# Performance work log

Hardware: AMD Instinct MI355X
Metric: run time of the kernel (lower is better)

## Reference

```python
import jax, jax.numpy as jnp
import numpy as np

B, SQ, SK = 2, 2048, 4096
D_STATE, D_LISTEN, D_PROJ, H = 512, 512, 512, 8


def setup_inputs() -> dict:
    key = jax.random.key(0)
    ks = jax.random.split(key, 9)
    s = 0.02
    return {
        "q": jax.random.normal(ks[0], (B, SQ, D_STATE), jnp.float32),
        "k": jax.random.normal(ks[1], (B, SK, D_LISTEN), jnp.float32),
        "mask": jax.random.randint(ks[2], (B, SK), 0, 2, jnp.int32),
        "Wq": jax.random.normal(ks[3], (D_STATE, D_PROJ), jnp.float32) * s,
        "bq": jnp.zeros((D_PROJ,), jnp.float32),
        "Wk": jax.random.normal(ks[4], (D_LISTEN, D_PROJ), jnp.float32) * s,
        "bk": jnp.zeros((D_PROJ,), jnp.float32),
        "Wv": jax.random.normal(ks[5], (D_LISTEN, D_PROJ), jnp.float32) * s,
        "bv": jnp.zeros((D_PROJ,), jnp.float32),
    }


def reference(q, k, mask, Wq, bq, Wk, bk, Wv, bv):
    # projections
    qp = q @ Wq + bq                      # [B, SQ, D]
    kp = k @ Wk + bk                      # [B, SK, D]
    vp = k @ Wv + bv                      # [B, SK, D]
    W = D_PROJ // H                        # head width
    qh = qp.reshape(B, SQ, H, W).transpose(0, 2, 1, 3)  # [B,H,SQ,W]
    kh = kp.reshape(B, SK, H, W).transpose(0, 2, 1, 3)  # [B,H,SK,W]
    vh = vp.reshape(B, SK, H, W).transpose(0, 2, 1, 3)  # [B,H,SK,W]
    scores = jnp.einsum("bhqw,bhkw->bhqk", qh, kh) / np.sqrt(W).astype(np.float32)
    m = mask[:, None, None, :].astype(jnp.float32)       # [B,1,1,SK]
    scores = scores - 10000.0 * (1.0 - m)
    attn = jax.nn.softmax(scores, axis=-1)               # dropout=0 (eval)
    h = jnp.einsum("bhqk,bhkw->bhqw", attn, vh)          # [B,H,SQ,W]
    h = h.transpose(0, 2, 1, 3).reshape(B, SQ, D_PROJ)
    return h
```

## Files before the change

### kernel.cpp

```cpp
#include <hip/hip_runtime.h>
#include <hip/hip_bf16.h>


typedef short  s16x8 __attribute__((ext_vector_type(8)));
typedef short  s16x4 __attribute__((ext_vector_type(4)));
typedef float  f32x4 __attribute__((ext_vector_type(4)));
typedef float  f32x16 __attribute__((ext_vector_type(16)));
typedef unsigned int u32;
typedef unsigned int u32x4 __attribute__((ext_vector_type(4)));

__device__ __forceinline__ unsigned short f2bf(float x) {
    return __builtin_bit_cast(unsigned short, __float2bfloat16(x));
}
__device__ __forceinline__ void gload16(const void* g, void* lds) {
    __builtin_amdgcn_global_load_lds(
        (const __attribute__((address_space(1))) unsigned int*)g,
        (__attribute__((address_space(3))) unsigned int*)lds, 16, 0, 0);
}
__device__ __forceinline__ u32 cvtpk(float lo, float hi) {
    u32 r;
    asm("v_cvt_pk_bf16_f32 %0, %1, %2" : "=v"(r) : "v"(lo), "v"(hi));
    return r;
}

__global__ __launch_bounds__(256) void prep(
    const float* __restrict__ q, const float* __restrict__ k,
    const float* __restrict__ Wq, const float* __restrict__ Wk,
    const float* __restrict__ Wv, const int* __restrict__ mask,
    unsigned short* __restrict__ qbf, unsigned short* __restrict__ kbf,
    unsigned short* __restrict__ wtq, unsigned short* __restrict__ wtk,
    unsigned short* __restrict__ wtv, float* __restrict__ mskf)
{
    __shared__ float T[64][65];
    const int bid = blockIdx.x;
    const int tid = threadIdx.x;
    if (bid < 3072) {
        const float* src = bid < 1024 ? q : k;
        unsigned short* dst = bid < 1024 ? qbf : kbf;
        int i = (bid < 1024 ? bid : bid - 1024) * 256 + tid;
        float4 a = reinterpret_cast<const float4*>(src)[2 * i];
        float4 b = reinterpret_cast<const float4*>(src)[2 * i + 1];
        s16x8 o;
        o[0] = (short)f2bf(a.x); o[1] = (short)f2bf(a.y);
        o[2] = (short)f2bf(a.z); o[3] = (short)f2bf(a.w);
        o[4] = (short)f2bf(b.x); o[5] = (short)f2bf(b.y);
        o[6] = (short)f2bf(b.z); o[7] = (short)f2bf(b.w);
        reinterpret_cast<s16x8*>(dst)[i] = o;
    } else if (bid < 3264) {
        int t = bid - 3072;
        int z = t >> 6;
        int tt = t & 63;
        const float* W = z == 0 ? Wq : z == 1 ? Wk : Wv;
        unsigned short* D = z == 0 ? wtq : z == 1 ? wtk : wtv;
        const int k0 = (tt >> 3) * 64, n0 = (tt & 7) * 64;
        const int r = tid >> 2, cq = tid & 3;
        #pragma unroll
        for (int p = 0; p < 4; ++p) {
            int c = (cq + 4 * p) * 4;
            float4 v = *reinterpret_cast<const float4*>(
                &W[(size_t)(k0 + r) * 512 + n0 + c]);
            T[c + 0][r] = v.x; T[c + 1][r] = v.y;
            T[c + 2][r] = v.z; T[c + 3][r] = v.w;
        }
        __syncthreads();
        #pragma unroll
        for (int p = 0; p < 4; ++p) {
            int kc = (cq + 4 * p) * 4;
            s16x4 o;
            o[0] = (short)f2bf(T[r][kc + 0]);
            o[1] = (short)f2bf(T[r][kc + 1]);
            o[2] = (short)f2bf(T[r][kc + 2]);
            o[3] = (short)f2bf(T[r][kc + 3]);
            *reinterpret_cast<s16x4*>(&D[(size_t)(n0 + r) * 512 + k0 + kc]) = o;
        }
    } else {
        int i = (bid - 3264) * 2048 + tid * 8;
        int4 m0 = *reinterpret_cast<const int4*>(&mask[i]);
        int4 m1 = *reinterpret_cast<const int4*>(&mask[i + 4]);
        const float C = -14426.950408889634f;
        float4 f0, f1;
        f0.x = C * (1.f - (float)m0.x); f0.y = C * (1.f - (float)m0.y);
        f0.z = C * (1.f - (float)m0.z); f0.w = C * (1.f - (float)m0.w);
        f1.x = C * (1.f - (float)m1.x); f1.y = C * (1.f - (float)m1.y);
        f1.z = C * (1.f - (float)m1.z); f1.w = C * (1.f - (float)m1.w);
        *reinterpret_cast<float4*>(&mskf[i])     = f0;
        *reinterpret_cast<float4*>(&mskf[i + 4]) = f1;
    }
}

__global__ __launch_bounds__(256) void proj3(
    const unsigned short* __restrict__ qbf, const unsigned short* __restrict__ kbf,
    const unsigned short* __restrict__ wtq, const unsigned short* __restrict__ wtk,
    const unsigned short* __restrict__ wtv,
    const float* __restrict__ bq, const float* __restrict__ bk,
    const float* __restrict__ bv,
    unsigned short* __restrict__ qh, unsigned short* __restrict__ kh,
    unsigned short* __restrict__ vt)
{
    __shared__ unsigned short As[2][128 * 64];
    __shared__ unsigned short Bs[2][64 * 64];

    const int tid  = threadIdx.x;
    const int wv   = tid >> 6;
    const int lane = tid & 63;
    const int g    = lane >> 4;
    const int ln   = lane & 15;
    const int swz  = (ln & 7) << 3;

    const int id = blockIdx.x;
    const unsigned short *A, *Wt;
    const float* bias;
    unsigned short* dst;
    int S, trans, nb, mb;
    if (id < 256)      { A = qbf; Wt = wtq; bias = bq; dst = qh; S = 2048; trans = 0; nb = id & 7;         mb = id >> 3; }
    else if (id < 768) { A = kbf; Wt = wtk; bias = bk; dst = kh; S = 4096; trans = 0; nb = (id - 256) & 7; mb = (id - 256) >> 3; }
    else               { A = kbf; Wt = wtv; bias = bv; dst = vt; S = 4096; trans = 1; nb = (id - 768) & 7; mb = (id - 768) >> 3; }
    const int m0 = mb * 128, n0 = nb * 64;

    f32x4 acc[4][2];
    #pragma unroll
    for (int i = 0; i < 4; ++i)
        #pragma unroll
        for (int j = 0; j < 2; ++j) acc[i][j] = (f32x4)0.f;

    auto stage = [&](int bufn, int k0) {
        #pragma unroll
        for (int p = 0; p < 4; ++p) {
            int slot = p * 256 + tid;
            int row = slot >> 3, cb = slot & 7;
            int cbp = cb ^ (row & 7);
            gload16(&A[(size_t)(m0 + row) * 512 + k0 + cbp * 8], &As[bufn][slot * 8]);
        }
        #pragma unroll
        for (int p = 0; p < 2; ++p) {
            int slot = p * 256 + tid;
            int row = slot >> 3, cb = slot & 7;
            int cbp = cb ^ (row & 7);
            gload16(&Wt[(size_t)(n0 + row) * 512 + k0 + cbp * 8], &Bs[bufn][slot * 8]);
        }
    };

    stage(0, 0);
    __syncthreads();
    int buf = 0;
    for (int kk = 0; kk < 8; ++kk) {
        if (kk < 7) stage(buf ^ 1, (kk + 1) * 64);
        #pragma unroll
        for (int ks = 0; ks < 2; ++ks) {
            s16x8 fa[2], fb[4];
            #pragma unroll
            for (int mi = 0; mi < 2; ++mi)
                fa[mi] = *reinterpret_cast<const s16x8*>(
                    &As[buf][((wv * 32 + 16 * mi + ln) * 64 + ks * 32 + g * 8) ^ swz]);
            #pragma unroll
            for (int nj = 0; nj < 4; ++nj)
                fb[nj] = *reinterpret_cast<const s16x8*>(
                    &Bs[buf][((16 * nj + ln) * 64 + ks * 32 + g * 8) ^ swz]);
            if (!trans) {
                #pragma unroll
                for (int mi = 0; mi < 2; ++mi)
                    #pragma unroll
                    for (int nj = 0; nj < 4; ++nj)
                        acc[nj][mi] = __builtin_amdgcn_mfma_f32_16x16x32_bf16(
                            fa[mi], fb[nj], acc[nj][mi], 0, 0, 0);
            } else {
                #pragma unroll
                for (int nj = 0; nj < 4; ++nj)
                    #pragma unroll
                    for (int mi = 0; mi < 2; ++mi)
                        acc[nj][mi] = __builtin_amdgcn_mfma_f32_16x16x32_bf16(
                            fb[nj], fa[mi], acc[nj][mi], 0, 0, 0);
            }
        }
        __syncthreads();
        buf ^= 1;
    }

    const int h    = nb;
    const int bidx = m0 / S;
    const int s0   = m0 - bidx * S;

    if (!trans) {
        float bvv[4];
        #pragma unroll
        for (int nj = 0; nj < 4; ++nj) bvv[nj] = bias[n0 + 16 * nj + ln];
        unsigned short* base = dst + (size_t)(bidx * 8 + h) * S * 64;
        #pragma unroll
        for (int mi = 0; mi < 2; ++mi)
            #pragma unroll
            for (int r = 0; r < 4; ++r) {
                int s = s0 + wv * 32 + 16 * mi + 4 * g + r;
                #pragma unroll
                for (int nj = 0; nj < 4; ++nj)
                    base[(size_t)s * 64 + 16 * nj + ln] =
                        f2bf(acc[nj][mi][r] + bvv[nj]);
            }
    } else {
        unsigned short* base = dst + (size_t)(bidx * 8 + h) * 64 * (size_t)S;
        #pragma unroll
        for (int nj = 0; nj < 4; ++nj)
            #pragma unroll
            for (int r = 0; r < 4; ++r) {
                int w = 16 * nj + 4 * g + r;
                float bw = bias[n0 + w];
                #pragma unroll
                for (int mi = 0; mi < 2; ++mi)
                    base[(size_t)w * S + s0 + wv * 32 + 16 * mi + ln] =
                        f2bf(acc[nj][mi][r] + bw);
            }
    }
}

__global__ __launch_bounds__(512, 2) void attn5(
    const unsigned short* __restrict__ qh,
    const unsigned short* __restrict__ kh,
    const unsigned short* __restrict__ vt,
    const float* __restrict__ mskf,
    float* __restrict__ out)
{
    __shared__ float Ored[2][4][32][36];
    __shared__ float lw[2][2][4][32];

    const int tid  = threadIdx.x;
    const int wid  = tid >> 6;
    const int kq   = wid & 3;
    const int qg   = wid >> 2;
    const int lane = tid & 63;
    const int l31  = lane & 31;
    const int h32  = lane >> 5;

    const int id  = blockIdx.x;
    const int xcd = id & 7;
    const int j   = id >> 3;
    const int bh  = xcd * 2 + (j >> 4);
    const int qt  = j & 15;
    const int b   = bh >> 3;
    const int hh  = bh & 7;

    const unsigned short* Kp = kh + (size_t)bh * 4096 * 64
                               + (size_t)(kq * 32 + l31) * 64 + h32 * 8;
    const unsigned short* Vp0 = vt + (size_t)bh * 64 * 4096
                               + (size_t)(l31) * 4096 + kq * 32 + h32 * 8;
    const float* mp = mskf + b * 4096 + kq * 32 + h32 * 4;

    s16x8 Qf[2][4];
    {
        const unsigned short* Qb = qh + ((size_t)bh * 2048 + qt * 128 + qg * 64) * 64;
        #pragma unroll
        for (int qt2 = 0; qt2 < 2; ++qt2)
            #pragma unroll
            for (int ks = 0; ks < 4; ++ks)
                Qf[qt2][ks] = *reinterpret_cast<const s16x8*>(
                    &Qb[(size_t)(qt2 * 32 + l31) * 64 + ks * 16 + h32 * 8]);
    }

    f32x16 O[2][2];
    #pragma unroll
    for (int i = 0; i < 2; ++i)
        #pragma unroll
        for (int jj = 0; jj < 2; ++jj) O[i][jj] = (f32x16)0.f;
    float l_acc0 = 0.f, l_acc1 = 0.f;

    s16x8 kf[4], vf[4];
    float4 mk[4];

    auto loadK = [&](int t) {
        #pragma unroll
        for (int ks = 0; ks < 4; ++ks)
            kf[ks] = *reinterpret_cast<const s16x8*>(Kp + (size_t)t * 8192 + ks * 16);
    };
    auto loadV = [&](int t) {
        #pragma unroll
        for (int wt = 0; wt < 2; ++wt)
            #pragma unroll
            for (int t2 = 0; t2 < 2; ++t2)
                vf[wt * 2 + t2] = *reinterpret_cast<const s16x8*>(
                    Vp0 + (size_t)wt * 32 * 4096 + t * 128 + t2 * 16);
    };
    auto loadM = [&](int t) {
        #pragma unroll
        for (int m = 0; m < 4; ++m)
            mk[m] = *reinterpret_cast<const float4*>(mp + t * 128 + m * 8);
    };

    loadM(0); loadK(0); loadV(0);

    for (int t = 0; t < 32; ++t) {
        f32x16 S[2];
        S[0] = (f32x16)0.f; S[1] = (f32x16)0.f;
        __builtin_amdgcn_s_setprio(1);
        #pragma unroll
        for (int ks = 0; ks < 4; ++ks) {
            S[0] = __builtin_amdgcn_mfma_f32_32x32x16_bf16(kf[ks], Qf[0][ks], S[0], 0, 0, 0);
            S[1] = __builtin_amdgcn_mfma_f32_32x32x16_bf16(kf[ks], Qf[1][ks], S[1], 0, 0, 0);
        }
        __builtin_amdgcn_s_setprio(0);
        if (t < 31) loadK(t + 1);

        s16x8 pa[2][2];
        #pragma unroll
        for (int qt2 = 0; qt2 < 2; ++qt2) {
            float pp[16];
            #pragma unroll
            for (int r = 0; r < 16; ++r) {
                float mb_ = (r & 3) == 0 ? mk[r >> 2].x :
                            (r & 3) == 1 ? mk[r >> 2].y :
                            (r & 3) == 2 ? mk[r >> 2].z : mk[r >> 2].w;
                pp[r] = exp2f(fmaf(S[qt2][r], 0.18033688011112042f, mb_));
            }
            float ls = ((pp[0] + pp[1]) + (pp[2] + pp[3]))
                     + ((pp[4] + pp[5]) + (pp[6] + pp[7]))
                     + ((pp[8] + pp[9]) + (pp[10] + pp[11]))
                     + ((pp[12] + pp[13]) + (pp[14] + pp[15]));
            if (qt2 == 0) l_acc0 += ls; else l_acc1 += ls;
            u32 W[8];
            #pragma unroll
            for (int c = 0; c < 4; ++c) {
                W[2 * c + 0] = cvtpk(pp[4 * c + 0], pp[4 * c + 1]);
                W[2 * c + 1] = cvtpk(pp[4 * c + 2], pp[4 * c + 3]);
            }
            asm("v_permlane32_swap_b32 %0, %1" : "+v"(W[0]), "+v"(W[2]));
            asm("v_permlane32_swap_b32 %0, %1" : "+v"(W[1]), "+v"(W[3]));
            asm("v_permlane32_swap_b32 %0, %1" : "+v"(W[4]), "+v"(W[6]));
            asm("v_permlane32_swap_b32 %0, %1" : "+v"(W[5]), "+v"(W[7]));
            u32x4 lo, hi;
            lo[0] = W[0]; lo[1] = W[1]; lo[2] = W[2]; lo[3] = W[3];
            hi[0] = W[4]; hi[1] = W[5]; hi[2] = W[6]; hi[3] = W[7];
            pa[qt2][0] = __builtin_bit_cast(s16x8, lo);
            pa[qt2][1] = __builtin_bit_cast(s16x8, hi);
        }

        __builtin_amdgcn_s_setprio(1);
        #pragma unroll
        for (int qt2 = 0; qt2 < 2; ++qt2)
            #pragma unroll
            for (int wt = 0; wt < 2; ++wt)
                #pragma unroll
                for (int t2 = 0; t2 < 2; ++t2)
                    O[qt2][wt] = __builtin_amdgcn_mfma_f32_32x32x16_bf16(
                        pa[qt2][t2], vf[wt * 2 + t2], O[qt2][wt], 0, 0, 0);
        __builtin_amdgcn_s_setprio(0);
        if (t < 31) { loadV(t + 1); loadM(t + 1); }
    }

    float ls0 = l_acc0 + __shfl_xor(l_acc0, 32);
    float ls1 = l_acc1 + __shfl_xor(l_acc1, 32);
    if (lane < 32) {
        lw[qg][0][kq][l31] = ls0;
        lw[qg][1][kq][l31] = ls1;
    }

    const int grp = tid >> 8;
    const int tt  = tid & 255;
    const int qr  = tt >> 3;
    const int w8  = (tt & 7) * 4;
    #pragma unroll
    for (int qt2 = 0; qt2 < 2; ++qt2)
        #pragma unroll
        for (int wt = 0; wt < 2; ++wt) {
            __syncthreads();
            f32x16 oo = O[qt2][wt];
            #pragma unroll
            for (int r = 0; r < 16; ++r)
                Ored[qg][kq][(r & 3) + 8 * (r >> 2) + 4 * h32][l31] = oo[r];
            __syncthreads();
            float4 s = *reinterpret_cast<const float4*>(&Ored[grp][0][qr][w8]);
            float4 s1 = *reinterpret_cast<const float4*>(&Ored[grp][1][qr][w8]);
            float4 s2 = *reinterpret_cast<const float4*>(&Ored[grp][2][qr][w8]);
            float4 s3 = *reinterpret_cast<const float4*>(&Ored[grp][3][qr][w8]);
            s.x += s1.x + s2.x + s3.x;
            s.y += s1.y + s2.y + s3.y;
            s.z += s1.z + s2.z + s3.z;
            s.w += s1.w + s2.w + s3.w;
            float l = lw[grp][qt2][0][qr] + lw[grp][qt2][1][qr]
                    + lw[grp][qt2][2][qr] + lw[grp][qt2][3][qr];
            float inv = 1.f / l;
            int qglob = qt * 128 + grp * 64 + qt2 * 32 + qr;
            float4 o;
            o.x = s.x * inv; o.y = s.y * inv; o.z = s.z * inv; o.w = s.w * inv;
            *reinterpret_cast<float4*>(
                &out[((size_t)b * 2048 + qglob) * 512 + hh * 64 + wt * 32 + w8]) = o;
        }
}

extern "C" void kernel_launch(void* const* d_in, const int* in_sizes, int n_in,
                              void* d_out, int out_size, void* d_ws, size_t ws_size,
                              hipStream_t stream)
{
    const float* q    = (const float*)d_in[0];
    const float* k    = (const float*)d_in[1];
    const int*   mask = (const int*)  d_in[2];
    const float* Wq   = (const float*)d_in[3];
    const float* bq   = (const float*)d_in[4];
    const float* Wk   = (const float*)d_in[5];
    const float* bk   = (const float*)d_in[6];
    const float* Wv   = (const float*)d_in[7];
    const float* bv   = (const float*)d_in[8];
    float* out = (float*)d_out;

    unsigned short* p = (unsigned short*)d_ws;
    unsigned short* qh  = p; p += (size_t)2 * 8 * 2048 * 64;
    unsigned short* kh  = p; p += (size_t)2 * 8 * 4096 * 64;
    unsigned short* vt  = p; p += (size_t)2 * 8 * 4096 * 64;
    unsigned short* qbf = p; p += (size_t)2 * 2048 * 512;
    unsigned short* kbf = p; p += (size_t)2 * 4096 * 512;
    unsigned short* wtq = p; p += 512 * 512;
    unsigned short* wtk = p; p += 512 * 512;
    unsigned short* wtv = p; p += 512 * 512;
    float* mskf = (float*)p;

    dim3 blk(256);
    prep<<<dim3(3268), blk, 0, stream>>>(q, k, Wq, Wk, Wv, mask,
                                         qbf, kbf, wtq, wtk, wtv, mskf);
    proj3<<<dim3(1280), blk, 0, stream>>>(qbf, kbf, wtq, wtk, wtv,
                                          bq, bk, bv, qh, kh, vt);
    attn5<<<dim3(256), dim3(512), 0, stream>>>(qh, kh, vt, mskf, out);
}
```

Measured before the change: 113.7 us.

## Halve query tile per block and double grid to raise occupancy in attention

The attention kernel now handles 64 query rows per block instead of 128, with each wave holding one 32-row Q tile instead of two. The grid goes from 256 to 512 blocks and launch bounds allow 4 blocks per CU. This cuts per-wave register use and gives more parallelism and latency hiding across the 256 CUs. In exchange, K and V reuse per load drops by half, so twice as much K/V traffic goes through the caches, and there is less independent MFMA work per wave to overlap with the softmax.

Result: slower. 172.9 us (+52.1%).

```diff
diff --git a/kernel.cpp b/kernel.cpp
--- a/kernel.cpp
+++ b/kernel.cpp
@@ -211,7 +211,7 @@
     }
 }
 
-__global__ __launch_bounds__(512, 2) void attn5(
+__global__ __launch_bounds__(512, 4) void attn6(
     const unsigned short* __restrict__ qh,
     const unsigned short* __restrict__ kh,
     const unsigned short* __restrict__ vt,
@@ -219,7 +219,7 @@
     float* __restrict__ out)
 {
     __shared__ float Ored[2][4][32][36];
-    __shared__ float lw[2][2][4][32];
+    __shared__ float lw[2][4][32];
 
     const int tid  = threadIdx.x;
     const int wid  = tid >> 6;
@@ -232,34 +232,29 @@
     const int id  = blockIdx.x;
     const int xcd = id & 7;
     const int j   = id >> 3;
-    const int bh  = xcd * 2 + (j >> 4);
-    const int qt  = j & 15;
+    const int bh  = xcd * 2 + (j >> 5);
+    const int qt  = j & 31;
     const int b   = bh >> 3;
     const int hh  = bh & 7;
 
     const unsigned short* Kp = kh + (size_t)bh * 4096 * 64
                                + (size_t)(kq * 32 + l31) * 64 + h32 * 8;
     const unsigned short* Vp0 = vt + (size_t)bh * 64 * 4096
-                               + (size_t)(l31) * 4096 + kq * 32 + h32 * 8;
+                               + (size_t)l31 * 4096 + kq * 32 + h32 * 8;
     const float* mp = mskf + b * 4096 + kq * 32 + h32 * 4;
 
-    s16x8 Qf[2][4];
+    s16x8 Qf[4];
     {
-        const unsigned short* Qb = qh + ((size_t)bh * 2048 + qt * 128 + qg * 64) * 64;
-        #pragma unroll
-        for (int qt2 = 0; qt2 < 2; ++qt2)
-            #pragma unroll
-            for (int ks = 0; ks < 4; ++ks)
-                Qf[qt2][ks] = *reinterpret_cast<const s16x8*>(
-                    &Qb[(size_t)(qt2 * 32 + l31) * 64 + ks * 16 + h32 * 8]);
-    }
-
-    f32x16 O[2][2];
-    #pragma unroll
-    for (int i = 0; i < 2; ++i)
-        #pragma unroll
-        for (int jj = 0; jj < 2; ++jj) O[i][jj] = (f32x16)0.f;
-    float l_acc0 = 0.f, l_acc1 = 0.f;
+        const unsigned short* Qb = qh + ((size_t)bh * 2048 + qt * 64 + qg * 32) * 64;
+        #pragma unroll
+        for (int ks = 0; ks < 4; ++ks)
+            Qf[ks] = *reinterpret_cast<const s16x8*>(
+                &Qb[(size_t)l31 * 64 + ks * 16 + h32 * 8]);
+    }
+
+    f32x16 O[2];
+    O[0] = (f32x16)0.f; O[1] = (f32x16)0.f;
+    float l_acc = 0.f;
 
     s16x8 kf[4], vf[4];
     float4 mk[4];
@@ -286,101 +281,86 @@
     loadM(0); loadK(0); loadV(0);
 
     for (int t = 0; t < 32; ++t) {
-        f32x16 S[2];
-        S[0] = (f32x16)0.f; S[1] = (f32x16)0.f;
+        f32x16 S = (f32x16)0.f;
         __builtin_amdgcn_s_setprio(1);
         #pragma unroll
-        for (int ks = 0; ks < 4; ++ks) {
-            S[0] = __builtin_amdgcn_mfma_f32_32x32x16_bf16(kf[ks], Qf[0][ks], S[0], 0, 0, 0);
-            S[1] = __builtin_amdgcn_mfma_f32_32x32x16_bf16(kf[ks], Qf[1][ks], S[1], 0, 0, 0);
-        }
+        for (int ks = 0; ks < 4; ++ks)
+            S = __builtin_amdgcn_mfma_f32_32x32x16_bf16(kf[ks], Qf[ks], S, 0, 0, 0);
         __builtin_amdgcn_s_setprio(0);
         if (t < 31) loadK(t + 1);
 
-        s16x8 pa[2][2];
-        #pragma unroll
-        for (int qt2 = 0; qt2 < 2; ++qt2) {
-            float pp[16];
-            #pragma unroll
-            for (int r = 0; r < 16; ++r) {
-                float mb_ = (r & 3) == 0 ? mk[r >> 2].x :
-                            (r & 3) == 1 ? mk[r >> 2].y :
-                            (r & 3) == 2 ? mk[r >> 2].z : mk[r >> 2].w;
-                pp[r] = exp2f(fmaf(S[qt2][r], 0.18033688011112042f, mb_));
-            }
-            float ls = ((pp[0] + pp[1]) + (pp[2] + pp[3]))
-                     + ((pp[4] + pp[5]) + (pp[6] + pp[7]))
-                     + ((pp[8] + pp[9]) + (pp[10] + pp[11]))
-                     + ((pp[12] + pp[13]) + (pp[14] + pp[15]));
-            if (qt2 == 0) l_acc0 += ls; else l_acc1 += ls;
-            u32 W[8];
-            #pragma unroll
-            for (int c = 0; c < 4; ++c) {
-                W[2 * c + 0] = cvtpk(pp[4 * c + 0], pp[4 * c + 1]);
-                W[2 * c + 1] = cvtpk(pp[4 * c + 2], pp[4 * c + 3]);
-            }
-            asm("v_permlane32_swap_b32 %0, %1" : "+v"(W[0]), "+v"(W[2]));
-            asm("v_permlane32_swap_b32 %0, %1" : "+v"(W[1]), "+v"(W[3]));
-            asm("v_permlane32_swap_b32 %0, %1" : "+v"(W[4]), "+v"(W[6]));
-            asm("v_permlane32_swap_b32 %0, %1" : "+v"(W[5]), "+v"(W[7]));
+        float pp[16];
+        #pragma unroll
+        for (int r = 0; r < 16; ++r) {
+            float mb_ = (r & 3) == 0 ? mk[r >> 2].x :
+                        (r & 3) == 1 ? mk[r >> 2].y :
+                        (r & 3) == 2 ? mk[r >> 2].z : mk[r >> 2].w;
+            pp[r] = exp2f(fmaf(S[r], 0.18033688011112042f, mb_));
+        }
+        l_acc += (((pp[0] + pp[1]) + (pp[2] + pp[3]))
+                + ((pp[4] + pp[5]) + (pp[6] + pp[7])))
+               + (((pp[8] + pp[9]) + (pp[10] + pp[11]))
+                + ((pp[12] + pp[13]) + (pp[14] + pp[15])));
+        if (t < 31) loadM(t + 1);
+        u32 W[8];
+        #pragma unroll
+        for (int c = 0; c < 4; ++c) {
+            W[2 * c + 0] = cvtpk(pp[4 * c + 0], pp[4 * c + 1]);
+            W[2 * c + 1] = cvtpk(pp[4 * c + 2], pp[4 * c + 3]);
+        }
+        asm("v_permlane32_swap_b32 %0, %1" : "+v"(W[0]), "+v"(W[2]));
+        asm("v_permlane32_swap_b32 %0, %1" : "+v"(W[1]), "+v"(W[3]));
+        asm("v_permlane32_swap_b32 %0, %1" : "+v"(W[4]), "+v"(W[6]));
+        asm("v_permlane32_swap_b32 %0, %1" : "+v"(W[5]), "+v"(W[7]));
+        s16x8 pa[2];
+        {
             u32x4 lo, hi;
             lo[0] = W[0]; lo[1] = W[1]; lo[2] = W[2]; lo[3] = W[3];
             hi[0] = W[4]; hi[1] = W[5]; hi[2] = W[6]; hi[3] = W[7];
-            pa[qt2][0] = __builtin_bit_cast(s16x8, lo);
-            pa[qt2][1] = __builtin_bit_cast(s16x8, hi);
+            pa[0] = __builtin_bit_cast(s16x8, lo);
+            pa[1] = __builtin_bit_cast(s16x8, hi);
         }
 
         __builtin_amdgcn_s_setprio(1);
         #pragma unroll
-        for (int qt2 = 0; qt2 < 2; ++qt2)
-            #pragma unroll
-            for (int wt = 0; wt < 2; ++wt)
-                #pragma unroll
-                for (int t2 = 0; t2 < 2; ++t2)
-                    O[qt2][wt] = __builtin_amdgcn_mfma_f32_32x32x16_bf16(
-                        pa[qt2][t2], vf[wt * 2 + t2], O[qt2][wt], 0, 0, 0);
+        for (int wt = 0; wt < 2; ++wt)
+            #pragma unroll
+            for (int t2 = 0; t2 < 2; ++t2)
+                O[wt] = __builtin_amdgcn_mfma_f32_32x32x16_bf16(
+                    pa[t2], vf[wt * 2 + t2], O[wt], 0, 0, 0);
         __builtin_amdgcn_s_setprio(0);
-        if (t < 31) { loadV(t + 1); loadM(t + 1); }
-    }
-
-    float ls0 = l_acc0 + __shfl_xor(l_acc0, 32);
-    float ls1 = l_acc1 + __shfl_xor(l_acc1, 32);
-    if (lane < 32) {
-        lw[qg][0][kq][l31] = ls0;
-        lw[qg][1][kq][l31] = ls1;
-    }
+        if (t < 31) loadV(t + 1);
+    }
+
+    float ls = l_acc + __shfl_xor(l_acc, 32);
+    if (lane < 32) lw[qg][kq][l31] = ls;
 
     const int grp = tid >> 8;
     const int tt  = tid & 255;
     const int qr  = tt >> 3;
     const int w8  = (tt & 7) * 4;
     #pragma unroll
-    for (int qt2 = 0; qt2 < 2; ++qt2)
-        #pragma unroll
-        for (int wt = 0; wt < 2; ++wt) {
-            __syncthreads();
-            f32x16 oo = O[qt2][wt];
-            #pragma unroll
-            for (int r = 0; r < 16; ++r)
-                Ored[qg][kq][(r & 3) + 8 * (r >> 2) + 4 * h32][l31] = oo[r];
-            __syncthreads();
-            float4 s = *reinterpret_cast<const float4*>(&Ored[grp][0][qr][w8]);
-            float4 s1 = *reinterpret_cast<const float4*>(&Ored[grp][1][qr][w8]);
-            float4 s2 = *reinterpret_cast<const float4*>(&Ored[grp][2][qr][w8]);
-            float4 s3 = *reinterpret_cast<const float4*>(&Ored[grp][3][qr][w8]);
-            s.x += s1.x + s2.x + s3.x;
-            s.y += s1.y + s2.y + s3.y;
-            s.z += s1.z + s2.z + s3.z;
-            s.w += s1.w + s2.w + s3.w;
-            float l = lw[grp][qt2][0][qr] + lw[grp][qt2][1][qr]
-                    + lw[grp][qt2][2][qr] + lw[grp][qt2][3][qr];
-            float inv = 1.f / l;
-            int qglob = qt * 128 + grp * 64 + qt2 * 32 + qr;
-            float4 o;
-            o.x = s.x * inv; o.y = s.y * inv; o.z = s.z * inv; o.w = s.w * inv;
-            *reinterpret_cast<float4*>(
-                &out[((size_t)b * 2048 + qglob) * 512 + hh * 64 + wt * 32 + w8]) = o;
-        }
+    for (int wt = 0; wt < 2; ++wt) {
+        __syncthreads();
+        #pragma unroll
+        for (int r = 0; r < 16; ++r)
+            Ored[qg][kq][(r & 3) + 8 * (r >> 2) + 4 * h32][l31] = O[wt][r];
+        __syncthreads();
+        float4 s0 = *reinterpret_cast<const float4*>(&Ored[grp][0][qr][w8]);
+        float4 s1 = *reinterpret_cast<const float4*>(&Ored[grp][1][qr][w8]);
+        float4 s2 = *reinterpret_cast<const float4*>(&Ored[grp][2][qr][w8]);
+        float4 s3 = *reinterpret_cast<const float4*>(&Ored[grp][3][qr][w8]);
+        float l = lw[grp][0][qr] + lw[grp][1][qr] + lw[grp][2][qr] + lw[grp][3][qr];
+        float inv = 1.f / l;
+        int qglob = qt * 64 + grp * 32 + qr;
+        float4 o;
+        o.x = (s0.x + s1.x + s2.x + s3.x) * inv;
+        o.y = (s0.y + s1.y + s2.y + s3.y) * inv;
+        o.z = (s0.z + s1.z + s2.z + s3.z) * inv;
+        o.w = (s0.w + s1.w + s2.w + s3.w) * inv;
+        *reinterpret_cast<float4*>(
+            &out[((size_t)b * 2048 + qglob) * 512 + hh * 64 + wt * 32 + w8]) = o;
+    }
 }
 
 extern "C" void kernel_launch(void* const* d_in, const int* in_sizes, int n_in,
@@ -414,5 +394,5 @@
                                          qbf, kbf, wtq, wtk, wtv, mskf);
     proj3<<<dim3(1280), blk, 0, stream>>>(qbf, kbf, wtq, wtk, wtv,
                                           bq, bk, bv, qh, kh, vt);
-    attn5<<<dim3(256), dim3(512), 0, stream>>>(qh, kh, vt, mskf, out);
-}
+    attn6<<<dim3(512), dim3(512), 0, stream>>>(qh, kh, vt, mskf, out);
+}
```
